# Optimization experiments

Measured on AMD Instinct MI355X. Metric: run time of the kernel, lower is better.

Reference implementation:

```python
import jax, jax.numpy as jnp
import numpy as np

N_NODES = 50000
NNZ = 800000
HYPER_DIM = 128
N_LAYERS = 2
LEAKY = 0.2
LN_EPS = 1e-5


def setup_inputs() -> dict:
    key = jax.random.key(0)
    k1, k2, k3, k4 = jax.random.split(key, 4)
    return {
        "ego_embeddings": jax.random.normal(k1, (N_NODES, HYPER_DIM), dtype=jnp.float32),
        "adj_vals": jax.random.uniform(k2, (NNZ,), dtype=jnp.float32),
        "ln_gamma": jnp.ones((N_LAYERS, HYPER_DIM), dtype=jnp.float32),
        "ln_beta": jnp.zeros((N_LAYERS, HYPER_DIM), dtype=jnp.float32),
        "adj_rows": jax.random.randint(k3, (NNZ,), 0, N_NODES, dtype=jnp.int32),
        "adj_cols": jax.random.randint(k4, (NNZ,), 0, N_NODES, dtype=jnp.int32),
        "n_users": 25000,
    }


def _spmm(rows, cols, vals, x, n_out):
    # y = A @ x for sparse A in COO (rows, cols, vals): gather + segment-sum
    return jax.ops.segment_sum(vals[:, None] * x[cols], rows, num_segments=n_out)


def _layer_norm(x, gamma, beta):
    mu = jnp.mean(x, axis=-1, keepdims=True)
    var = jnp.mean(jnp.square(x - mu), axis=-1, keepdims=True)
    return (x - mu) * jax.lax.rsqrt(var + LN_EPS) * gamma + beta


def reference(ego_embeddings, adj_vals, ln_gamma, ln_beta, adj_rows, adj_cols, n_users):
    res = ego_embeddings
    embs = ego_embeddings
    for k in range(N_LAYERS):
        # adj.T @ embs  (rows of A^T are cols of A)
        ht = _spmm(adj_cols, adj_rows, adj_vals, embs, N_NODES)
        # adj @ (adj.T @ embs)
        h = _spmm(adj_rows, adj_cols, adj_vals, ht, N_NODES)
        if k != N_LAYERS - 1:
            h = jnp.where(h >= 0, h, LEAKY * h)  # LeakyReLU
        embs = _layer_norm(h, ln_gamma[k], ln_beta[k]) + res
    user_emb = embs[:n_users]
    item_emb = embs[n_users:]
    return (user_emb, item_emb)
```

## Files before the change

### kernel.cpp

```cpp
#include <hip/hip_runtime.h>
#include <hip/hip_bf16.h>

#define HD 128
#define PB 256
#define NBA 256
#define LEAKY 0.2f
#define LN_EPS 1e-5f

__device__ __forceinline__ unsigned short bfr(float f) {
    unsigned int b = __float_as_uint(f);
    return (unsigned short)((b + 0x7fffu + ((b >> 16) & 1u)) >> 16);
}
__device__ __forceinline__ float blo(unsigned int u) { return __uint_as_float(u << 16); }
__device__ __forceinline__ float bhi(unsigned int u) { return __uint_as_float(u & 0xffff0000u); }

__global__ __launch_bounds__(256) void f32_to_bf16(
    const float* __restrict__ x, unsigned short* __restrict__ y, int n4) {
    int i = blockIdx.x * 256 + threadIdx.x;
    if (i >= n4) return;
    float4 f = ((const float4*)x)[i];
    ushort4 u;
    u.x = bfr(f.x); u.y = bfr(f.y); u.z = bfr(f.z); u.w = bfr(f.w);
    ((ushort4*)y)[i] = u;
}


__global__ __launch_bounds__(256) void part_count(
    const int* __restrict__ rows, const int* __restrict__ cols,
    int* __restrict__ counts, int nnz) {
    __shared__ int cR[NBA], cC[NBA];
    cR[threadIdx.x] = 0; cC[threadIdx.x] = 0;
    __syncthreads();
    int chunk = (nnz + PB - 1) / PB;
    int beg = blockIdx.x * chunk;
    int end = min(beg + chunk, nnz);
    for (int i = beg + threadIdx.x; i < end; i += 256) {
        atomicAdd(&cR[rows[i] >> 8], 1);
        atomicAdd(&cC[cols[i] >> 8], 1);
    }
    __syncthreads();
    counts[(size_t)blockIdx.x * NBA + threadIdx.x] = cR[threadIdx.x];
    counts[(size_t)PB * NBA + (size_t)blockIdx.x * NBA + threadIdx.x] = cC[threadIdx.x];
}

__global__ __launch_bounds__(64) void part_off(
    int* __restrict__ counts, int* __restrict__ totals) {
    int bkt = blockIdx.x, dir = blockIdx.y, lane = threadIdx.x;
    int* p = counts + (size_t)dir * PB * NBA;
    int v[4], s = 0;
    #pragma unroll
    for (int j = 0; j < 4; ++j) {
        int blk = lane * 4 + j;
        v[j] = p[(size_t)blk * NBA + bkt];
        s += v[j];
    }
    int incl = s;
    #pragma unroll
    for (int off = 1; off < 64; off <<= 1) {
        int t = __shfl_up(incl, off);
        if (lane >= off) incl += t;
    }
    int excl = incl - s;
    #pragma unroll
    for (int j = 0; j < 4; ++j) {
        int blk = lane * 4 + j;
        p[(size_t)blk * NBA + bkt] = excl;
        excl += v[j];
    }
    if (lane == 63) totals[dir * NBA + bkt] = incl;
}

__global__ __launch_bounds__(128) void base_scan(
    const int* __restrict__ totals, int* __restrict__ bases,
    int* __restrict__ rp_r, int* __restrict__ rp_c, int nbk, int n, int nnz) {
    int dir = threadIdx.x >> 6, lane = threadIdx.x & 63;
    int v[4], s = 0;
    #pragma unroll
    for (int j = 0; j < 4; ++j) {
        int b = lane * 4 + j;
        v[j] = (b < nbk) ? totals[dir * NBA + b] : 0;
        s += v[j];
    }
    int incl = s;
    #pragma unroll
    for (int off = 1; off < 64; off <<= 1) {
        int t = __shfl_up(incl, off);
        if (lane >= off) incl += t;
    }
    int excl = incl - s;
    #pragma unroll
    for (int j = 0; j < 4; ++j) {
        bases[dir * NBA + lane * 4 + j] = excl;
        excl += v[j];
    }
    if (lane == 0) (dir ? rp_c : rp_r)[n] = nnz;
}

__global__ __launch_bounds__(256) void part_scatter(
    const int* __restrict__ rows, const int* __restrict__ cols,
    const float* __restrict__ vals,
    const int* __restrict__ counts, const int* __restrict__ bases,
    uint2* __restrict__ stg_r, uint2* __restrict__ stg_c, int nnz) {
    __shared__ int cR[NBA], cC[NBA], wbR[NBA], wbC[NBA];
    int t = threadIdx.x;
    cR[t] = 0; cC[t] = 0;
    wbR[t] = bases[t] + counts[(size_t)blockIdx.x * NBA + t];
    wbC[t] = bases[NBA + t] + counts[(size_t)PB * NBA + (size_t)blockIdx.x * NBA + t];
    __syncthreads();
    int chunk = (nnz + PB - 1) / PB;
    int beg = blockIdx.x * chunk;
    int end = min(beg + chunk, nnz);
    for (int i = beg + threadIdx.x; i < end; i += 256) {
        int ro = rows[i], co = cols[i];
        unsigned vb = (unsigned)bfr(vals[i]) << 16;
        int rk = atomicAdd(&cR[ro >> 8], 1);
        stg_r[wbR[ro >> 8] + rk] = make_uint2(vb | (unsigned)co, (unsigned)ro);
        int ck = atomicAdd(&cC[co >> 8], 1);
        stg_c[wbC[co >> 8] + ck] = make_uint2(vb | (unsigned)ro, (unsigned)co);
    }
}

__global__ __launch_bounds__(1024) void bucket_build(
    const uint2* __restrict__ stg_r, const uint2* __restrict__ stg_c,
    const int* __restrict__ totals, const int* __restrict__ bases,
    unsigned* __restrict__ ent_r, unsigned* __restrict__ ent_c,
    int* __restrict__ rp_r, int* __restrict__ rp_c, int n) {
    __shared__ int cnt[NBA];
    __shared__ int wsum[4], woff[4];
    int bkt = blockIdx.x, dir = blockIdx.y;
    const uint2* stg = dir ? stg_c : stg_r;
    unsigned* ent = dir ? ent_c : ent_r;
    int* rp = dir ? rp_c : rp_r;
    int base = bases[dir * NBA + bkt];
    int total = totals[dir * NBA + bkt];
    int lo = bkt << 8;
    int nb = min(NBA, n - lo);
    int tid = threadIdx.x;
    if (tid < NBA) cnt[tid] = 0;
    __syncthreads();
    for (int i = tid; i < total; i += 1024)
        atomicAdd(&cnt[(int)stg[base + i].y - lo], 1);
    __syncthreads();
    int lane = tid & 63, wid = tid >> 6;
    int v = (tid < NBA) ? cnt[tid] : 0;
    int incl = v;
    #pragma unroll
    for (int off = 1; off < 64; off <<= 1) {
        int t = __shfl_up(incl, off);
        if (lane >= off) incl += t;
    }
    if (lane == 63 && wid < 4) wsum[wid] = incl;
    __syncthreads();
    if (tid == 0) {
        int run = 0;
        #pragma unroll
        for (int w = 0; w < 4; ++w) { woff[w] = run; run += wsum[w]; }
    }
    __syncthreads();
    if (tid < NBA) {
        int excl = woff[wid] + incl - v;
        if (tid < nb) rp[lo + tid] = base + excl;
        cnt[tid] = excl;
    }
    __syncthreads();
    for (int i = tid; i < total; i += 1024) {
        uint2 e = stg[base + i];
        int pos = atomicAdd(&cnt[(int)e.y - lo], 1);
        ent[base + pos] = e.x;
    }
}

__global__ __launch_bounds__(256) void spmm_bf(
    const unsigned short* __restrict__ x, const int* __restrict__ rp,
    const unsigned* __restrict__ ent,
    const float* __restrict__ res, const float* __restrict__ gamma,
    const float* __restrict__ beta,
    unsigned short* __restrict__ out_bf, float* __restrict__ out_f32,
    int n, int post) {
    int wid = threadIdx.x >> 6, lane = threadIdx.x & 63;
    int row = blockIdx.x * 4 + wid;
    if (row >= n) return;
    int quarter = lane >> 4, q = lane & 15;
    int beg = rp[row], end = rp[row + 1];
    float acc[8];
    #pragma unroll
    for (int k = 0; k < 8; ++k) acc[k] = 0.f;

    int last = end - 1;
    for (int i0 = beg + quarter; i0 < end; i0 += 16) {
        int i1 = i0 + 4, i2 = i0 + 8, i3 = i0 + 12;
        unsigned e0 = ent[i0];
        unsigned e1 = ent[i1 < end ? i1 : last];
        unsigned e2 = ent[i2 < end ? i2 : last];
        unsigned e3 = ent[i3 < end ? i3 : last];
        uint4 u0 = ((const uint4*)(x + (size_t)(e0 & 0xffffu) * HD))[q];
        uint4 u1 = ((const uint4*)(x + (size_t)(e1 & 0xffffu) * HD))[q];
        uint4 u2 = ((const uint4*)(x + (size_t)(e2 & 0xffffu) * HD))[q];
        uint4 u3 = ((const uint4*)(x + (size_t)(e3 & 0xffffu) * HD))[q];
        float v0 = bhi(e0);
        float v1 = i1 < end ? bhi(e1) : 0.f;
        float v2 = i2 < end ? bhi(e2) : 0.f;
        float v3 = i3 < end ? bhi(e3) : 0.f;
        acc[0] += v0 * blo(u0.x) + v1 * blo(u1.x);
        acc[1] += v0 * bhi(u0.x) + v1 * bhi(u1.x);
        acc[2] += v0 * blo(u0.y) + v1 * blo(u1.y);
        acc[3] += v0 * bhi(u0.y) + v1 * bhi(u1.y);
        acc[4] += v0 * blo(u0.z) + v1 * blo(u1.z);
        acc[5] += v0 * bhi(u0.z) + v1 * bhi(u1.z);
        acc[6] += v0 * blo(u0.w) + v1 * blo(u1.w);
        acc[7] += v0 * bhi(u0.w) + v1 * bhi(u1.w);
        acc[0] += v2 * blo(u2.x) + v3 * blo(u3.x);
        acc[1] += v2 * bhi(u2.x) + v3 * bhi(u3.x);
        acc[2] += v2 * blo(u2.y) + v3 * blo(u3.y);
        acc[3] += v2 * bhi(u2.y) + v3 * bhi(u3.y);
        acc[4] += v2 * blo(u2.z) + v3 * blo(u3.z);
        acc[5] += v2 * bhi(u2.z) + v3 * bhi(u3.z);
        acc[6] += v2 * blo(u2.w) + v3 * blo(u3.w);
        acc[7] += v2 * bhi(u2.w) + v3 * bhi(u3.w);
    }
    #pragma unroll
    for (int k = 0; k < 8; ++k) {
        acc[k] += __shfl_xor(acc[k], 16);
        acc[k] += __shfl_xor(acc[k], 32);
    }
    if (quarter != 0) return;

    if (post == 0) {
        uint4 s;
        s.x = (unsigned)bfr(acc[0]) | ((unsigned)bfr(acc[1]) << 16);
        s.y = (unsigned)bfr(acc[2]) | ((unsigned)bfr(acc[3]) << 16);
        s.z = (unsigned)bfr(acc[4]) | ((unsigned)bfr(acc[5]) << 16);
        s.w = (unsigned)bfr(acc[6]) | ((unsigned)bfr(acc[7]) << 16);
        ((uint4*)(out_bf + (size_t)row * HD))[q] = s;
        return;
    }
    if (post == 1) {
        #pragma unroll
        for (int k = 0; k < 8; ++k) acc[k] = acc[k] >= 0.f ? acc[k] : LEAKY * acc[k];
    }
    float t = 0.f;
    #pragma unroll
    for (int k = 0; k < 8; ++k) t += acc[k];
    #pragma unroll
    for (int off = 1; off < 16; off <<= 1) t += __shfl_xor(t, off);
    float mu = t * (1.f / HD);
    float d[8], vs = 0.f;
    #pragma unroll
    for (int k = 0; k < 8; ++k) { d[k] = acc[k] - mu; vs += d[k] * d[k]; }
    #pragma unroll
    for (int off = 1; off < 16; off <<= 1) vs += __shfl_xor(vs, off);
    float inv = rsqrtf(vs * (1.f / HD) + LN_EPS);

    float4 g0 = ((const float4*)gamma)[2 * q], g1 = ((const float4*)gamma)[2 * q + 1];
    float4 b0 = ((const float4*)beta)[2 * q],  b1 = ((const float4*)beta)[2 * q + 1];
    float4 r0 = ((const float4*)(res + (size_t)row * HD))[2 * q];
    float4 r1 = ((const float4*)(res + (size_t)row * HD))[2 * q + 1];
    float o[8];
    o[0] = d[0] * inv * g0.x + b0.x + r0.x;
    o[1] = d[1] * inv * g0.y + b0.y + r0.y;
    o[2] = d[2] * inv * g0.z + b0.z + r0.z;
    o[3] = d[3] * inv * g0.w + b0.w + r0.w;
    o[4] = d[4] * inv * g1.x + b1.x + r1.x;
    o[5] = d[5] * inv * g1.y + b1.y + r1.y;
    o[6] = d[6] * inv * g1.z + b1.z + r1.z;
    o[7] = d[7] * inv * g1.w + b1.w + r1.w;
    if (post == 1) {
        uint4 s;
        s.x = (unsigned)bfr(o[0]) | ((unsigned)bfr(o[1]) << 16);
        s.y = (unsigned)bfr(o[2]) | ((unsigned)bfr(o[3]) << 16);
        s.z = (unsigned)bfr(o[4]) | ((unsigned)bfr(o[5]) << 16);
        s.w = (unsigned)bfr(o[6]) | ((unsigned)bfr(o[7]) << 16);
        ((uint4*)(out_bf + (size_t)row * HD))[q] = s;
    } else {
        float4 s0 = {o[0], o[1], o[2], o[3]};
        float4 s1 = {o[4], o[5], o[6], o[7]};
        ((float4*)(out_f32 + (size_t)row * HD))[2 * q] = s0;
        ((float4*)(out_f32 + (size_t)row * HD))[2 * q + 1] = s1;
    }
}

extern "C" void kernel_launch(void* const* d_in, const int* in_sizes, int n_in,
                              void* d_out, int out_size, void* d_ws, size_t ws_size,
                              hipStream_t stream) {
    const float* ego   = (const float*)d_in[0];
    const float* vals  = (const float*)d_in[1];
    const float* gamma = (const float*)d_in[2];
    const float* beta  = (const float*)d_in[3];
    const int*   rows  = (const int*)d_in[4];
    const int*   cols  = (const int*)d_in[5];

    const int N   = in_sizes[0] / HD;
    const int NNZ = in_sizes[1];
    const int NBK = (N + 255) >> 8;

    float* out = (float*)d_out;
    char* w = (char*)d_ws;
    unsigned short* ego_bf = (unsigned short*)w; w += (size_t)N * HD * 2;
    unsigned short* bufA   = (unsigned short*)w; w += (size_t)N * HD * 2;
    unsigned short* bufB   = (unsigned short*)w; w += (size_t)N * HD * 2;
    int*  rp_r = (int*)w;  w += (size_t)(N + 4) * 4;
    int*  rp_c = (int*)w;  w += (size_t)(N + 4) * 4;
    unsigned* ent_r = (unsigned*)w; w += (size_t)NNZ * 4;
    unsigned* ent_c = (unsigned*)w; w += (size_t)NNZ * 4;
    int* counts = (int*)w; w += (size_t)2 * PB * NBA * 4;
    int* totals = (int*)w; w += (size_t)2 * NBA * 4;
    int* bases  = (int*)w; w += (size_t)2 * NBA * 4;

    uint2* stg_r = (uint2*)bufB;
    uint2* stg_c = stg_r + NNZ;

    f32_to_bf16<<<(N * HD / 4 + 255) / 256, 256, 0, stream>>>(ego, ego_bf, N * HD / 4);
    part_count<<<PB, 256, 0, stream>>>(rows, cols, counts, NNZ);
    part_off<<<dim3(NBK, 2), 64, 0, stream>>>(counts, totals);
    base_scan<<<1, 128, 0, stream>>>(totals, bases, rp_r, rp_c, NBK, N, NNZ);
    part_scatter<<<PB, 256, 0, stream>>>(rows, cols, vals, counts, bases,
                                         stg_r, stg_c, NNZ);
    bucket_build<<<dim3(NBK, 2), 1024, 0, stream>>>(stg_r, stg_c, totals, bases,
                                                    ent_r, ent_c, rp_r, rp_c, N);

    const int sblocks = (N + 3) / 4;

    spmm_bf<<<sblocks, 256, 0, stream>>>(ego_bf, rp_c, ent_c,
                                         nullptr, nullptr, nullptr, bufA, nullptr, N, 0);
    spmm_bf<<<sblocks, 256, 0, stream>>>(bufA, rp_r, ent_r,
                                         ego, gamma, beta, bufB, nullptr, N, 1);
    spmm_bf<<<sblocks, 256, 0, stream>>>(bufB, rp_c, ent_c,
                                         nullptr, nullptr, nullptr, bufA, nullptr, N, 0);
    spmm_bf<<<sblocks, 256, 0, stream>>>(bufA, rp_r, ent_r,
                                         ego, gamma + HD, beta + HD, nullptr, out, N, 2);
}
```

Measured before the change: 250.4 us.

## Replace two-pass bucket partition CSR build with global-atomic degree count and direct scatter

The CSR/CSC build is rewritten. A two-level bucket partition (per-block bucket counts, staged uint2 scatter, per-bucket local sort) is replaced by per-node degree counting with global atomics, a block-wise prefix scan plus bucket bases, and a direct scatter using global atomic cursors. The goal is to drop the staging buffer pass and the bucket_build kernel, and the bf16 conversion is fused with zeroing the degree arrays. The cost is many contended global atomics and nondeterministic entry order within each row, so floating-point summation order varies between runs.

```diff
diff --git a/kernel.cpp b/kernel.cpp
--- a/kernel.cpp
+++ b/kernel.cpp
@@ -2,7 +2,6 @@
 #include <hip/hip_bf16.h>
 
 #define HD 128
-#define PB 256
 #define NBA 256
 #define LEAKY 0.2f
 #define LN_EPS 1e-5f
@@ -14,60 +13,65 @@
 __device__ __forceinline__ float blo(unsigned int u) { return __uint_as_float(u << 16); }
 __device__ __forceinline__ float bhi(unsigned int u) { return __uint_as_float(u & 0xffff0000u); }
 
-__global__ __launch_bounds__(256) void f32_to_bf16(
-    const float* __restrict__ x, unsigned short* __restrict__ y, int n4) {
-    int i = blockIdx.x * 256 + threadIdx.x;
-    if (i >= n4) return;
-    float4 f = ((const float4*)x)[i];
-    ushort4 u;
-    u.x = bfr(f.x); u.y = bfr(f.y); u.z = bfr(f.z); u.w = bfr(f.w);
-    ((ushort4*)y)[i] = u;
-}
-
-
-__global__ __launch_bounds__(256) void part_count(
+__global__ __launch_bounds__(256) void conv_zero(
+    const float* __restrict__ x, unsigned short* __restrict__ y, int n4,
+    int* __restrict__ deg, int ndeg) {
+    int stride = gridDim.x * 256;
+    for (int i = blockIdx.x * 256 + threadIdx.x; i < n4; i += stride) {
+        float4 f = ((const float4*)x)[i];
+        ushort4 u;
+        u.x = bfr(f.x); u.y = bfr(f.y); u.z = bfr(f.z); u.w = bfr(f.w);
+        ((ushort4*)y)[i] = u;
+    }
+    for (int i = blockIdx.x * 256 + threadIdx.x; i < ndeg; i += stride)
+        deg[i] = 0;
+}
+
+__global__ __launch_bounds__(256) void count_deg(
     const int* __restrict__ rows, const int* __restrict__ cols,
-    int* __restrict__ counts, int nnz) {
-    __shared__ int cR[NBA], cC[NBA];
-    cR[threadIdx.x] = 0; cC[threadIdx.x] = 0;
-    __syncthreads();
-    int chunk = (nnz + PB - 1) / PB;
-    int beg = blockIdx.x * chunk;
-    int end = min(beg + chunk, nnz);
-    for (int i = beg + threadIdx.x; i < end; i += 256) {
-        atomicAdd(&cR[rows[i] >> 8], 1);
-        atomicAdd(&cC[cols[i] >> 8], 1);
-    }
-    __syncthreads();
-    counts[(size_t)blockIdx.x * NBA + threadIdx.x] = cR[threadIdx.x];
-    counts[(size_t)PB * NBA + (size_t)blockIdx.x * NBA + threadIdx.x] = cC[threadIdx.x];
-}
-
-__global__ __launch_bounds__(64) void part_off(
-    int* __restrict__ counts, int* __restrict__ totals) {
-    int bkt = blockIdx.x, dir = blockIdx.y, lane = threadIdx.x;
-    int* p = counts + (size_t)dir * PB * NBA;
-    int v[4], s = 0;
-    #pragma unroll
-    for (int j = 0; j < 4; ++j) {
-        int blk = lane * 4 + j;
-        v[j] = p[(size_t)blk * NBA + bkt];
-        s += v[j];
-    }
-    int incl = s;
+    int* __restrict__ deg_r, int* __restrict__ deg_c, int nnz) {
+    int stride = gridDim.x * 256;
+    int t = blockIdx.x * 256 + threadIdx.x;
+    int n4 = nnz >> 2;
+    for (int j = t; j < n4; j += stride) {
+        int4 r = ((const int4*)rows)[j];
+        int4 c = ((const int4*)cols)[j];
+        atomicAdd(&deg_r[r.x], 1); atomicAdd(&deg_r[r.y], 1);
+        atomicAdd(&deg_r[r.z], 1); atomicAdd(&deg_r[r.w], 1);
+        atomicAdd(&deg_c[c.x], 1); atomicAdd(&deg_c[c.y], 1);
+        atomicAdd(&deg_c[c.z], 1); atomicAdd(&deg_c[c.w], 1);
+    }
+    for (int j = (n4 << 2) + t; j < nnz; j += stride) {
+        atomicAdd(&deg_r[rows[j]], 1);
+        atomicAdd(&deg_c[cols[j]], 1);
+    }
+}
+
+__global__ __launch_bounds__(256) void bucket_sums(
+    const int* __restrict__ deg_r, const int* __restrict__ deg_c,
+    int* __restrict__ rp_r, int* __restrict__ rp_c,
+    int* __restrict__ totals, int n) {
+    __shared__ int wsum[4];
+    int bkt = blockIdx.x, dir = blockIdx.y, tid = threadIdx.x;
+    const int* deg = dir ? deg_c : deg_r;
+    int* rp = dir ? rp_c : rp_r;
+    int g = (bkt << 8) + tid;
+    int v = (g < n) ? deg[g] : 0;
+    int lane = tid & 63, wid = tid >> 6;
+    int incl = v;
     #pragma unroll
     for (int off = 1; off < 64; off <<= 1) {
         int t = __shfl_up(incl, off);
         if (lane >= off) incl += t;
     }
-    int excl = incl - s;
-    #pragma unroll
-    for (int j = 0; j < 4; ++j) {
-        int blk = lane * 4 + j;
-        p[(size_t)blk * NBA + bkt] = excl;
-        excl += v[j];
-    }
-    if (lane == 63) totals[dir * NBA + bkt] = incl;
+    if (lane == 63) wsum[wid] = incl;
+    __syncthreads();
+    int wbase = 0;
+    #pragma unroll
+    for (int w = 0; w < 4; ++w) if (w < wid) wbase += wsum[w];
+    int excl = wbase + incl - v;
+    if (g < n) rp[g] = excl;
+    if (tid == 255) totals[dir * NBA + bkt] = wbase + incl;
 }
 
 __global__ __launch_bounds__(128) void base_scan(
@@ -96,77 +100,33 @@
     if (lane == 0) (dir ? rp_c : rp_r)[n] = nnz;
 }
 
-__global__ __launch_bounds__(256) void part_scatter(
+__global__ __launch_bounds__(256) void add_base(
+    const int* __restrict__ bases,
+    int* __restrict__ rp_r, int* __restrict__ rp_c,
+    int* __restrict__ cur_r, int* __restrict__ cur_c, int n) {
+    int bkt = blockIdx.x, dir = blockIdx.y, tid = threadIdx.x;
+    int g = (bkt << 8) + tid;
+    if (g >= n) return;
+    int* rp = dir ? rp_c : rp_r;
+    int* cur = dir ? cur_c : cur_r;
+    int v = rp[g] + bases[dir * NBA + bkt];
+    rp[g] = v;
+    cur[g] = v;
+}
+
+__global__ __launch_bounds__(256) void scatter_direct(
     const int* __restrict__ rows, const int* __restrict__ cols,
     const float* __restrict__ vals,
-    const int* __restrict__ counts, const int* __restrict__ bases,
-    uint2* __restrict__ stg_r, uint2* __restrict__ stg_c, int nnz) {
-    __shared__ int cR[NBA], cC[NBA], wbR[NBA], wbC[NBA];
-    int t = threadIdx.x;
-    cR[t] = 0; cC[t] = 0;
-    wbR[t] = bases[t] + counts[(size_t)blockIdx.x * NBA + t];
-    wbC[t] = bases[NBA + t] + counts[(size_t)PB * NBA + (size_t)blockIdx.x * NBA + t];
-    __syncthreads();
-    int chunk = (nnz + PB - 1) / PB;
-    int beg = blockIdx.x * chunk;
-    int end = min(beg + chunk, nnz);
-    for (int i = beg + threadIdx.x; i < end; i += 256) {
+    int* __restrict__ cur_r, int* __restrict__ cur_c,
+    unsigned* __restrict__ ent_r, unsigned* __restrict__ ent_c, int nnz) {
+    int stride = gridDim.x * 256;
+    for (int i = blockIdx.x * 256 + threadIdx.x; i < nnz; i += stride) {
         int ro = rows[i], co = cols[i];
         unsigned vb = (unsigned)bfr(vals[i]) << 16;
-        int rk = atomicAdd(&cR[ro >> 8], 1);
-        stg_r[wbR[ro >> 8] + rk] = make_uint2(vb | (unsigned)co, (unsigned)ro);
-        int ck = atomicAdd(&cC[co >> 8], 1);
-        stg_c[wbC[co >> 8] + ck] = make_uint2(vb | (unsigned)ro, (unsigned)co);
-    }
-}
-
-__global__ __launch_bounds__(1024) void bucket_build(
-    const uint2* __restrict__ stg_r, const uint2* __restrict__ stg_c,
-    const int* __restrict__ totals, const int* __restrict__ bases,
-    unsigned* __restrict__ ent_r, unsigned* __restrict__ ent_c,
-    int* __restrict__ rp_r, int* __restrict__ rp_c, int n) {
-    __shared__ int cnt[NBA];
-    __shared__ int wsum[4], woff[4];
-    int bkt = blockIdx.x, dir = blockIdx.y;
-    const uint2* stg = dir ? stg_c : stg_r;
-    unsigned* ent = dir ? ent_c : ent_r;
-    int* rp = dir ? rp_c : rp_r;
-    int base = bases[dir * NBA + bkt];
-    int total = totals[dir * NBA + bkt];
-    int lo = bkt << 8;
-    int nb = min(NBA, n - lo);
-    int tid = threadIdx.x;
-    if (tid < NBA) cnt[tid] = 0;
-    __syncthreads();
-    for (int i = tid; i < total; i += 1024)
-        atomicAdd(&cnt[(int)stg[base + i].y - lo], 1);
-    __syncthreads();
-    int lane = tid & 63, wid = tid >> 6;
-    int v = (tid < NBA) ? cnt[tid] : 0;
-    int incl = v;
-    #pragma unroll
-    for (int off = 1; off < 64; off <<= 1) {
-        int t = __shfl_up(incl, off);
-        if (lane >= off) incl += t;
-    }
-    if (lane == 63 && wid < 4) wsum[wid] = incl;
-    __syncthreads();
-    if (tid == 0) {
-        int run = 0;
-        #pragma unroll
-        for (int w = 0; w < 4; ++w) { woff[w] = run; run += wsum[w]; }
-    }
-    __syncthreads();
-    if (tid < NBA) {
-        int excl = woff[wid] + incl - v;
-        if (tid < nb) rp[lo + tid] = base + excl;
-        cnt[tid] = excl;
-    }
-    __syncthreads();
-    for (int i = tid; i < total; i += 1024) {
-        uint2 e = stg[base + i];
-        int pos = atomicAdd(&cnt[(int)e.y - lo], 1);
-        ent[base + pos] = e.x;
+        int pr = atomicAdd(&cur_r[ro], 1);
+        ent_r[pr] = vb | (unsigned)co;
+        int pc = atomicAdd(&cur_c[co], 1);
+        ent_c[pc] = vb | (unsigned)ro;
     }
 }
 
@@ -302,21 +262,21 @@
     int*  rp_c = (int*)w;  w += (size_t)(N + 4) * 4;
     unsigned* ent_r = (unsigned*)w; w += (size_t)NNZ * 4;
     unsigned* ent_c = (unsigned*)w; w += (size_t)NNZ * 4;
-    int* counts = (int*)w; w += (size_t)2 * PB * NBA * 4;
+    int* deg_r = (int*)w;  w += (size_t)N * 4;
+    int* deg_c = (int*)w;  w += (size_t)N * 4;
+    int* cur_r = (int*)w;  w += (size_t)N * 4;
+    int* cur_c = (int*)w;  w += (size_t)N * 4;
     int* totals = (int*)w; w += (size_t)2 * NBA * 4;
     int* bases  = (int*)w; w += (size_t)2 * NBA * 4;
 
-    uint2* stg_r = (uint2*)bufB;
-    uint2* stg_c = stg_r + NNZ;
-
-    f32_to_bf16<<<(N * HD / 4 + 255) / 256, 256, 0, stream>>>(ego, ego_bf, N * HD / 4);
-    part_count<<<PB, 256, 0, stream>>>(rows, cols, counts, NNZ);
-    part_off<<<dim3(NBK, 2), 64, 0, stream>>>(counts, totals);
+    conv_zero<<<2048, 256, 0, stream>>>(ego, ego_bf, N * HD / 4, deg_r, 2 * N);
+    count_deg<<<1024, 256, 0, stream>>>(rows, cols, deg_r, deg_c, NNZ);
+    bucket_sums<<<dim3(NBK, 2), 256, 0, stream>>>(deg_r, deg_c, rp_r, rp_c,
+                                                  totals, N);
     base_scan<<<1, 128, 0, stream>>>(totals, bases, rp_r, rp_c, NBK, N, NNZ);
-    part_scatter<<<PB, 256, 0, stream>>>(rows, cols, vals, counts, bases,
-                                         stg_r, stg_c, NNZ);
-    bucket_build<<<dim3(NBK, 2), 1024, 0, stream>>>(stg_r, stg_c, totals, bases,
-                                                    ent_r, ent_c, rp_r, rp_c, N);
+    add_base<<<dim3(NBK, 2), 256, 0, stream>>>(bases, rp_r, rp_c, cur_r, cur_c, N);
+    scatter_direct<<<1024, 256, 0, stream>>>(rows, cols, vals, cur_r, cur_c,
+                                             ent_r, ent_c, NNZ);
 
     const int sblocks = (N + 3) / 4;
 
```

Result: slower. 400.3 us (+59.9%).
